# Kernel tuning notes

Hardware: AMD Instinct MI355X
Metric: run time of the kernel (lower is better)

The kernel has to match this reference:

```python
import jax, jax.numpy as jnp
import numpy as np

NUM_CLUSTER = 64
NUM_HEAD = 8
EMBED = 512
B, L = 32, 256
H = EMBED // NUM_HEAD  # 64


def setup_inputs() -> dict:
    key = jax.random.key(0)
    ks = jax.random.split(key, 8)
    inputs = jax.random.normal(ks[0], (B, L, EMBED), dtype=jnp.float32)
    emissions = jax.random.normal(ks[1], (B, L, NUM_CLUSTER), dtype=jnp.float32)
    targets = jax.random.randint(ks[2], (B, L), 0, NUM_CLUSTER)
    masks = jnp.ones((B, L), dtype=bool)
    scale = 1.0 / np.sqrt(H)
    W1 = jax.random.normal(ks[3], (NUM_CLUSTER, H), dtype=jnp.float32) * scale
    b1 = jax.random.normal(ks[4], (NUM_CLUSTER,), dtype=jnp.float32) * 0.01
    W2 = jax.random.normal(ks[5], (NUM_CLUSTER, H), dtype=jnp.float32) * scale
    b2 = jax.random.normal(ks[6], (NUM_CLUSTER,), dtype=jnp.float32) * 0.01
    start_transitions = jax.random.uniform(ks[7], (NUM_CLUSTER,), minval=-0.1, maxval=0.1, dtype=jnp.float32)
    end_transitions = jax.random.uniform(jax.random.fold_in(key, 99), (NUM_CLUSTER,), minval=-0.1, maxval=0.1, dtype=jnp.float32)
    return {"inputs": inputs, "emissions": emissions, "targets": targets, "masks": masks,
            "W1": W1, "b1": b1, "W2": W2, "b2": b2,
            "start_transitions": start_transitions, "end_transitions": end_transitions}


def reference(inputs, emissions, targets, masks, W1, b1, W2, b2, start_transitions, end_transitions):
    # batch_first -> time-major (L, B, ...)
    x = jnp.transpose(inputs, (1, 0, 2))          # [L,B,D]
    em = jnp.transpose(emissions, (1, 0, 2))      # [L,B,K]
    tg = targets.T                                # [L,B]
    mk = masks.T                                  # [L,B] bool
    Ls, Bs, D = x.shape
    K = start_transitions.shape[0]

    # biaffine per-step transitions: [L,B,K,K]
    flat = x.reshape(Ls, Bs, NUM_HEAD, D // NUM_HEAD)        # [L,B,C,H]
    e1 = jnp.einsum('lbch,kh->lbck', flat, W1) + b1          # [L,B,C,K]
    e2 = jnp.einsum('lbch,kh->lbck', flat, W2) + b2
    T = jnp.einsum('lbck,lbcj->lbkj', e1, e2)                # sum over channels

    mf = mk.astype(em.dtype)
    barange = jnp.arange(Bs)

    # ---- numerator (gold path score) ----
    score = start_transitions[tg[0]] + em[0, barange, tg[0]]
    steps = jnp.arange(1, Ls)[:, None]                       # [L-1,1]
    trans_sel = T[steps, barange[None, :], tg[:-1], tg[1:]]  # [L-1,B]
    em_sel = em[steps, barange[None, :], tg[1:]]             # [L-1,B]
    score = score + jnp.sum((trans_sel + em_sel) * mf[1:], axis=0)
    seq_ends = mk.astype(jnp.int32).sum(axis=0) - 1
    last_tags = tg[seq_ends, barange]
    numerator = score + end_transitions[last_tags]

    # ---- denominator (log partition) via scan ----
    def step(s, inp):
        Ti, emi, mki = inp                                   # [B,K,K],[B,K],[B]
        nxt = jax.nn.logsumexp(s[:, :, None] + Ti + emi[:, None, :], axis=1)
        s = jnp.where(mki[:, None], nxt, s)
        return s, None

    s0 = start_transitions + em[0]                           # [B,K]
    sF, _ = jax.lax.scan(step, s0, (T[1:], em[1:], mk[1:]))
    denominator = jax.nn.logsumexp(sF + end_transitions, axis=1)

    return numerator - denominator
```

## Files before the change

### kernel.cpp

```cpp
#include <hip/hip_runtime.h>
#include <hip/hip_bf16.h>
#include <cstddef>
#include <cstdint>

constexpr int Bn = 32;
constexpr int Ln = 256;
constexpr int SCH = 16;
constexpr int NCH = 16;

using bf16 = __hip_bfloat16;
typedef __bf16 bfv8 __attribute__((ext_vector_type(8)));
typedef float f32x16 __attribute__((ext_vector_type(16)));

union FragU {
  bfv8 f;
  uint4 q;
  uint2 d[2];
  unsigned short u[8];
};

__device__ inline unsigned int packbf2(float a, float b) {
  unsigned short lo = __builtin_bit_cast(unsigned short, __float2bfloat16(a));
  unsigned short hi = __builtin_bit_cast(unsigned short, __float2bfloat16(b));
  return (unsigned int)lo | ((unsigned int)hi << 16);
}
__device__ inline float bfbits2f(unsigned short v) {
  return __builtin_bit_cast(float, ((unsigned int)v) << 16);
}

__global__ __launch_bounds__(256) void chunk_kernel(
    const float* __restrict__ x, const float* __restrict__ W1,
    const float* __restrict__ b1, const float* __restrict__ W2,
    const float* __restrict__ b2, const float* __restrict__ em,
    const int* __restrict__ tg, bf16* __restrict__ cM,
    float* __restrict__ cOff, float* __restrict__ pnum) {
  const int blk = blockIdx.x;
  const int b = blk & (Bn - 1);
  const int c = blk >> 5;
  const int tid = threadIdx.x;
  const int lane = tid & 63;
  const int wv = tid >> 6;
  const int l31 = lane & 31, h5 = lane >> 5;

  __shared__ __align__(16) unsigned short smem[34816];
  __shared__ __align__(16) float ems[SCH * 64];
  __shared__ float wvoff[4], w2off[2];

  unsigned short* e1s = smem;
  unsigned short* e2s = smem + 8192;

  const int t0g = c * SCH;

  {
    const float4* src = (const float4*)(em + ((size_t)b * Ln + t0g) * 64);
    ((float4*)ems)[tid] = src[tid];
  }

  FragU fxa[4];
  {
    const float* xbase = x + ((size_t)(b * Ln + t0g)) * 512;
    const int m = wv * 32 + l31;
    const float* xrow = xbase + (size_t)(m >> 3) * 512 + (m & 7) * 64;
#pragma unroll
    for (int kb = 0; kb < 4; ++kb) {
      const float4 x0 = *(const float4*)(xrow + kb * 16 + h5 * 8);
      const float4 x1 = *(const float4*)(xrow + kb * 16 + h5 * 8 + 4);
      fxa[kb].d[0] = make_uint2(packbf2(x0.x, x0.y), packbf2(x0.z, x0.w));
      fxa[kb].d[1] = make_uint2(packbf2(x1.x, x1.y), packbf2(x1.z, x1.w));
    }
  }
#pragma unroll
  for (int arr = 0; arr < 2; ++arr) {
    const float* W = arr ? W2 : W1;
    const float* bb = arr ? b2 : b1;
    unsigned short* es = arr ? e2s : e1s;
#pragma unroll
    for (int nt = 0; nt < 2; ++nt) {
      const int k = nt * 32 + l31;
      f32x16 acc;
#pragma unroll
      for (int r = 0; r < 16; ++r) acc[r] = 0.f;
#pragma unroll
      for (int kb = 0; kb < 4; ++kb) {
        FragU fb;
        const float* wp = W + (size_t)k * 64 + kb * 16 + h5 * 8;
        const float4 w0 = *(const float4*)wp;
        const float4 w1 = *(const float4*)(wp + 4);
        fb.d[0] = make_uint2(packbf2(w0.x, w0.y), packbf2(w0.z, w0.w));
        fb.d[1] = make_uint2(packbf2(w1.x, w1.y), packbf2(w1.z, w1.w));
        acc = __builtin_amdgcn_mfma_f32_32x32x16_bf16(fxa[kb].f, fb.f, acc, 0, 0, 0);
      }
      const float bias = bb[k];
#pragma unroll
      for (int g = 0; g < 4; ++g) {
        const int tt = wv * 4 + g;
        const unsigned int lo = packbf2(acc[4 * g + 0] + bias, acc[4 * g + 1] + bias);
        const unsigned int hi = packbf2(acc[4 * g + 2] + bias, acc[4 * g + 3] + bias);
        *(uint2*)&es[tt * 512 + k * 8 + 4 * h5] = make_uint2(lo, hi);
      }
    }
  }
  __syncthreads();

  FragU f1[4][2], f2[4][2];
#pragma unroll
  for (int g = 0; g < 4; ++g)
#pragma unroll
    for (int a = 0; a < 2; ++a) {
      f1[g][a].q = make_uint4(0, 0, 0, 0);
      f2[g][a].q = make_uint4(0, 0, 0, 0);
      if (h5 == 0) {
        f1[g][a].q = *(const uint4*)&e1s[(4 * wv + g) * 512 + (a * 32 + l31) * 8];
        f2[g][a].q = *(const uint4*)&e2s[(4 * wv + g) * 512 + (a * 32 + l31) * 8];
      }
    }

  if (tid < 16) {
    const int tglob = t0g + tid;
    float part = 0.f;
    if (tglob >= 1) {
      const int kp = tg[b * Ln + tglob - 1];
      const int jc = tg[b * Ln + tglob];
      const unsigned short* p1 = &e1s[tid * 512 + kp * 8];
      const unsigned short* p2 = &e2s[tid * 512 + jc * 8];
      float tr = 0.f;
#pragma unroll
      for (int cc = 0; cc < 8; ++cc) tr += bfbits2f(p1[cc]) * bfbits2f(p2[cc]);
      part = tr + ems[tid * 64 + jc];
    }
#pragma unroll
    for (int o = 1; o < 16; o <<= 1) part += __shfl_xor(part, o);
    if (tid == 0) pnum[c * Bn + b] = part;
  }

  __syncthreads();

  unsigned short* A = smem + wv * 8704;
  unsigned short* Bs = A + 4352;

  auto wmax4 = [&](const f32x16& v0, const f32x16& v1, const f32x16& v2,
                   const f32x16& v3) -> float {
    float mx = v0[0];
#pragma unroll
    for (int r = 0; r < 16; ++r) {
      mx = fmaxf(mx, v0[r]); mx = fmaxf(mx, v1[r]);
      mx = fmaxf(mx, v2[r]); mx = fmaxf(mx, v3[r]);
    }
#pragma unroll
    for (int o = 1; o < 64; o <<= 1) mx = fmaxf(mx, __shfl_xor(mx, o));
    return mx;
  };

  auto stExp = [&](unsigned short* dst, const f32x16& v, int a2, int b2,
                   float sh) {
    unsigned short* d = &dst[(b2 * 32 + l31) * 68 + a2 * 32 + 4 * h5];
#pragma unroll
    for (int g = 0; g < 4; ++g) {
      const unsigned int lo =
          packbf2(__expf(v[4 * g + 0] - sh), __expf(v[4 * g + 1] - sh));
      const unsigned int hi =
          packbf2(__expf(v[4 * g + 2] - sh), __expf(v[4 * g + 3] - sh));
      *(uint2*)(d + 8 * g) = make_uint2(lo, hi);
    }
  };
  auto stScl = [&](unsigned short* dst, const f32x16& v, int a2, int b2,
                   float inv) {
    unsigned short* d = &dst[(b2 * 32 + l31) * 68 + a2 * 32 + 4 * h5];
#pragma unroll
    for (int g = 0; g < 4; ++g) {
      const unsigned int lo = packbf2(v[4 * g + 0] * inv, v[4 * g + 1] * inv);
      const unsigned int hi = packbf2(v[4 * g + 2] * inv, v[4 * g + 3] * inv);
      *(uint2*)(d + 8 * g) = make_uint2(lo, hi);
    }
  };

  auto computeP_R = [&](const FragU (&fe1)[2], const FragU (&fe2)[2], int tt,
                        unsigned short* dst) -> float {
    f32x16 c00, c01, c10, c11;
#pragma unroll
    for (int r = 0; r < 16; ++r) {
      const int rm = 4 * h5 + (r & 3) + 8 * (r >> 2);
      const float e0 = ems[tt * 64 + rm];
      const float e1v = ems[tt * 64 + 32 + rm];
      c00[r] = e0; c01[r] = e0; c10[r] = e1v; c11[r] = e1v;
    }
    c00 = __builtin_amdgcn_mfma_f32_32x32x16_bf16(fe2[0].f, fe1[0].f, c00, 0, 0, 0);
    c01 = __builtin_amdgcn_mfma_f32_32x32x16_bf16(fe2[0].f, fe1[1].f, c01, 0, 0, 0);
    c10 = __builtin_amdgcn_mfma_f32_32x32x16_bf16(fe2[1].f, fe1[0].f, c10, 0, 0, 0);
    c11 = __builtin_amdgcn_mfma_f32_32x32x16_bf16(fe2[1].f, fe1[1].f, c11, 0, 0, 0);
    const float mx = wmax4(c00, c01, c10, c11);
    stExp(dst, c00, 0, 0, mx);
    stExp(dst, c01, 0, 1, mx);
    stExp(dst, c10, 1, 0, mx);
    stExp(dst, c11, 1, 1, mx);
    return mx;
  };

  auto computeP_T = [&](const FragU (&fe1)[2], const FragU (&fe2)[2], int tt,
                        unsigned short* dst) -> float {
    const float emv0 = ems[tt * 64 + l31];
    const float emv1 = ems[tt * 64 + 32 + l31];
    f32x16 c00, c01, c10, c11;
#pragma unroll
    for (int r = 0; r < 16; ++r) {
      c00[r] = emv0; c01[r] = emv1; c10[r] = emv0; c11[r] = emv1;
    }
    c00 = __builtin_amdgcn_mfma_f32_32x32x16_bf16(fe1[0].f, fe2[0].f, c00, 0, 0, 0);
    c01 = __builtin_amdgcn_mfma_f32_32x32x16_bf16(fe1[0].f, fe2[1].f, c01, 0, 0, 0);
    c10 = __builtin_amdgcn_mfma_f32_32x32x16_bf16(fe1[1].f, fe2[0].f, c10, 0, 0, 0);
    c11 = __builtin_amdgcn_mfma_f32_32x32x16_bf16(fe1[1].f, fe2[1].f, c11, 0, 0, 0);
    const float mx = wmax4(c00, c01, c10, c11);
    stExp(dst, c00, 0, 0, mx);
    stExp(dst, c01, 0, 1, mx);
    stExp(dst, c10, 1, 0, mx);
    stExp(dst, c11, 1, 1, mx);
    return mx;
  };

  auto foldProd = [&](unsigned short* Adst, const unsigned short* Bsrc,
                      bool outT) -> float {
    const unsigned short* X = outT ? Adst : Bsrc;
    const unsigned short* Y = outT ? Bsrc : Adst;
    f32x16 a00, a01, a10, a11;
#pragma unroll
    for (int r = 0; r < 16; ++r) {
      a00[r] = 0.f; a01[r] = 0.f; a10[r] = 0.f; a11[r] = 0.f;
    }
#pragma unroll
    for (int kb = 0; kb < 4; ++kb) {
      const int koff = kb * 16 + h5 * 8;
      FragU x0, x1, y0, y1;
      const unsigned short* px0 = &X[l31 * 68 + koff];
      const unsigned short* px1 = &X[(32 + l31) * 68 + koff];
      const unsigned short* py0 = &Y[l31 * 68 + koff];
      const unsigned short* py1 = &Y[(32 + l31) * 68 + koff];
      x0.d[0] = *(const uint2*)px0;  x0.d[1] = *(const uint2*)(px0 + 4);
      x1.d[0] = *(const uint2*)px1;  x1.d[1] = *(const uint2*)(px1 + 4);
      y0.d[0] = *(const uint2*)py0;  y0.d[1] = *(const uint2*)(py0 + 4);
      y1.d[0] = *(const uint2*)py1;  y1.d[1] = *(const uint2*)(py1 + 4);
      a00 = __builtin_amdgcn_mfma_f32_32x32x16_bf16(x0.f, y0.f, a00, 0, 0, 0);
      a01 = __builtin_amdgcn_mfma_f32_32x32x16_bf16(x0.f, y1.f, a01, 0, 0, 0);
      a10 = __builtin_amdgcn_mfma_f32_32x32x16_bf16(x1.f, y0.f, a10, 0, 0, 0);
      a11 = __builtin_amdgcn_mfma_f32_32x32x16_bf16(x1.f, y1.f, a11, 0, 0, 0);
    }
    float mx = wmax4(a00, a01, a10, a11);
    mx = fmaxf(mx, 1e-30f);
    const float inv = 1.0f / mx;
    stScl(Adst, a00, 0, 0, inv);
    stScl(Adst, a01, 0, 1, inv);
    stScl(Adst, a10, 1, 0, inv);
    stScl(Adst, a11, 1, 1, inv);
    return __logf(mx);
  };

  float woff = 0.f;
  const int tstart = (c == 0 && wv == 0) ? 1 : 0;
  bool inited = false;
#pragma unroll
  for (int s = 0; s < 4; ++s) {
    if (s < tstart) continue;
    const int tt = 4 * wv + s;
    if (!inited) {
      woff += computeP_R(f1[s], f2[s], tt, A);
      inited = true;
    } else {
      woff += computeP_T(f1[s], f2[s], tt, Bs);
      woff += foldProd(A, Bs, (s == 3) && ((wv & 1) != 0));
    }
  }
  if (lane == 0) wvoff[wv] = woff;
  __syncthreads();

  if (wv == 0) {
    const float lm = foldProd(smem, smem + 8704, false);
    if (lane == 0) w2off[0] = wvoff[0] + wvoff[1] + lm;
  } else if (wv == 1) {
    const float lm = foldProd(smem + 2 * 8704, smem + 3 * 8704, true);
    if (lane == 0) w2off[1] = wvoff[2] + wvoff[3] + lm;
  }
  __syncthreads();

  if (wv == 0) {
    const float lm = foldProd(smem, smem + 2 * 8704, (c & 1) != 0);
    if (lane == 0) cOff[c * Bn + b] = w2off[0] + w2off[1] + lm;
  }
  __syncthreads();

  bf16* om = cM + ((size_t)(c * Bn + b)) * 4096;
#pragma unroll
  for (int pass = 0; pass < 4; ++pass) {
    const int e = pass * 1024 + tid * 4;
    const int i = e >> 6, j = e & 63;
    *(uint2*)((unsigned short*)om + e) = *(const uint2*)&smem[i * 68 + j];
  }
}

__global__ __launch_bounds__(256) void combine_kernel(
    const float* __restrict__ em, const int* __restrict__ tg,
    const float* __restrict__ st, const float* __restrict__ en,
    const bf16* __restrict__ cM, const float* __restrict__ cOff,
    const float* __restrict__ pnum, float* __restrict__ out) {
  const int b = blockIdx.x, tid = threadIdx.x;
  const int lane = tid & 63, wv = tid >> 6;
  const int l31 = lane & 31, h5 = lane >> 5;

  __shared__ __align__(16) unsigned short slots[8 * 4352];
  __shared__ float sexs[64];
  __shared__ float toff[8], toff2[4];
  __shared__ float num_s, den_s;

  float s0e = 0.f, env = 0.f, coffv = 0.f, pnv = 0.f;
  int tg0 = 0, tgl = 0;
  if (wv == 0) {
    s0e = __expf(st[lane] + em[(size_t)b * Ln * 64 + lane]);
    env = __expf(en[lane]);
    if (lane < 16) coffv = cOff[lane * Bn + b];
  } else if (wv == 1) {
    if (lane < 16) pnv = pnum[lane * Bn + b];
    if (lane == 0) {
      tg0 = tg[b * Ln];
      tgl = tg[b * Ln + Ln - 1];
    }
  }

  auto wmax4 = [&](const f32x16& v0, const f32x16& v1, const f32x16& v2,
                   const f32x16& v3) -> float {
    float mx = v0[0];
#pragma unroll
    for (int r = 0; r < 16; ++r) {
      mx = fmaxf(mx, v0[r]); mx = fmaxf(mx, v1[r]);
      mx = fmaxf(mx, v2[r]); mx = fmaxf(mx, v3[r]);
    }
#pragma unroll
    for (int o = 1; o < 64; o <<= 1) mx = fmaxf(mx, __shfl_xor(mx, o));
    return mx;
  };

  auto stTile = [&](unsigned short* dst, const f32x16& v, int i2, int j2,
                    float inv) {
    unsigned short* d = &dst[(j2 * 32 + l31) * 68 + i2 * 32 + 4 * h5];
#pragma unroll
    for (int g = 0; g < 4; ++g) {
      const unsigned int lo = packbf2(v[4 * g + 0] * inv, v[4 * g + 1] * inv);
      const unsigned int hi = packbf2(v[4 * g + 2] * inv, v[4 * g + 3] * inv);
      *(uint2*)(d + 8 * g) = make_uint2(lo, hi);
    }
  };

  auto prodL1 = [&](int pr) -> float {
    const unsigned short* Ag =
        (const unsigned short*)(cM + ((size_t)((2 * pr) * Bn + b)) * 4096);
    const unsigned short* Bg =
        (const unsigned short*)(cM + ((size_t)((2 * pr + 1) * Bn + b)) * 4096);
    const bool outT = (pr & 1) != 0;
    const unsigned short* X = outT ? Ag : Bg;
    const unsigned short* Y = outT ? Bg : Ag;
    f32x16 a00, a01, a10, a11;
#pragma unroll
    for (int r = 0; r < 16; ++r) {
      a00[r] = 0.f; a01[r] = 0.f; a10[r] = 0.f; a11[r] = 0.f;
    }
#pragma unroll
    for (int kb = 0; kb < 4; ++kb) {
      const int koff = kb * 16 + h5 * 8;
      FragU x0, x1, y0, y1;
      x0.q = *(const uint4*)&X[l31 * 64 + koff];
      x1.q = *(const uint4*)&X[(32 + l31) * 64 + koff];
      y0.q = *(const uint4*)&Y[l31 * 64 + koff];
      y1.q = *(const uint4*)&Y[(32 + l31) * 64 + koff];
      a00 = __builtin_amdgcn_mfma_f32_32x32x16_bf16(x0.f, y0.f, a00, 0, 0, 0);
      a01 = __builtin_amdgcn_mfma_f32_32x32x16_bf16(x0.f, y1.f, a01, 0, 0, 0);
      a10 = __builtin_amdgcn_mfma_f32_32x32x16_bf16(x1.f, y0.f, a10, 0, 0, 0);
      a11 = __builtin_amdgcn_mfma_f32_32x32x16_bf16(x1.f, y1.f, a11, 0, 0, 0);
    }
    float mx = wmax4(a00, a01, a10, a11);
    mx = fmaxf(mx, 1e-30f);
    const float inv = 1.0f / mx;
    unsigned short* dst = slots + pr * 4352;
    stTile(dst, a00, 0, 0, inv);
    stTile(dst, a01, 0, 1, inv);
    stTile(dst, a10, 1, 0, inv);
    stTile(dst, a11, 1, 1, inv);
    return __logf(mx);
  };

  auto prodL2 = [&](int q) -> float {
    const unsigned short* Xs = slots + (2 * q + 1) * 4352;
    const unsigned short* Ys = slots + (2 * q) * 4352;
    f32x16 a00, a01, a10, a11;
#pragma unroll
    for (int r = 0; r < 16; ++r) {
      a00[r] = 0.f; a01[r] = 0.f; a10[r] = 0.f; a11[r] = 0.f;
    }
#pragma unroll
    for (int kb = 0; kb < 4; ++kb) {
      const int koff = kb * 16 + h5 * 8;
      FragU x0, x1, y0, y1;
      const unsigned short* px0 = &Xs[l31 * 68 + koff];
      const unsigned short* px1 = &Xs[(32 + l31) * 68 + koff];
      const unsigned short* py0 = &Ys[l31 * 68 + koff];
      const unsigned short* py1 = &Ys[(32 + l31) * 68 + koff];
      x0.d[0] = *(const uint2*)px0;  x0.d[1] = *(const uint2*)(px0 + 4);
      x1.d[0] = *(const uint2*)px1;  x1.d[1] = *(const uint2*)(px1 + 4);
      y0.d[0] = *(const uint2*)py0;  y0.d[1] = *(const uint2*)(py0 + 4);
      y1.d[0] = *(const uint2*)py1;  y1.d[1] = *(const uint2*)(py1 + 4);
      a00 = __builtin_amdgcn_mfma_f32_32x32x16_bf16(x0.f, y0.f, a00, 0, 0, 0);
      a01 = __builtin_amdgcn_mfma_f32_32x32x16_bf16(x0.f, y1.f, a01, 0, 0, 0);
      a10 = __builtin_amdgcn_mfma_f32_32x32x16_bf16(x1.f, y0.f, a10, 0, 0, 0);
      a11 = __builtin_amdgcn_mfma_f32_32x32x16_bf16(x1.f, y1.f, a11, 0, 0, 0);
    }
    float mx = wmax4(a00, a01, a10, a11);
    mx = fmaxf(mx, 1e-30f);
    const float inv = 1.0f / mx;
    unsigned short* dst = slots + (2 * q) * 4352;
    stTile(dst, a00, 0, 0, inv);
    stTile(dst, a01, 0, 1, inv);
    stTile(dst, a10, 1, 0, inv);
    stTile(dst, a11, 1, 1, inv);
    return __logf(mx);
  };

#pragma unroll
  for (int pp = 0; pp < 2; ++pp) {
    const int pr = wv + pp * 4;
    const float lm = prodL1(pr);
    if (lane == 0) toff[pr] = lm;
  }
  __syncthreads();

  {
    const float child = toff[2 * wv] + toff[2 * wv + 1];
    const float lm2 = prodL2(wv);
    if (lane == 0) toff2[wv] = child + lm2;
  }
  __syncthreads();

  if (wv == 0) {
    float u = s0e;
#pragma unroll
    for (int f = 0; f < 4; ++f) {
      sexs[lane] = u;
      float acc2 = 0.f;
      const unsigned short* Mp = slots + (2 * f) * 4352;
#pragma unroll 8
      for (int k = 0; k < 64; ++k)
        acc2 += sexs[k] * bfbits2f(Mp[k * 68 + lane]);
      u = acc2;
    }
    const float w = u * env;
    float sg = w;
#pragma unroll
    for (int o = 1; o < 64; o <<= 1) sg += __shfl_xor(sg, o);
#pragma unroll
    for (int o = 1; o < 16; o <<= 1) coffv += __shfl_xor(coffv, o);
    if (lane == 0) {
      const float toffsum = toff2[0] + toff2[1] + toff2[2] + toff2[3];
      den_s = coffv + toffsum + __logf(sg);
    }
  } else if (wv == 1) {
    float nsum = pnv;
#pragma unroll
    for (int o = 1; o < 16; o <<= 1) nsum += __shfl_xor(nsum, o);
    if (lane == 0)
      num_s = nsum + st[tg0] + em[(size_t)b * Ln * 64 + tg0] + en[tgl];
  }
  __syncthreads();
  if (tid == 0) out[b] = num_s - den_s;
}

extern "C" void kernel_launch(void* const* d_in, const int* in_sizes, int n_in,
                              void* d_out, int out_size, void* d_ws, size_t ws_size,
                              hipStream_t stream) {
  const float* inputs    = (const float*)d_in[0];
  const float* emissions = (const float*)d_in[1];
  const int*   targets   = (const int*)d_in[2];
  const float* W1 = (const float*)d_in[4];
  const float* b1 = (const float*)d_in[5];
  const float* W2 = (const float*)d_in[6];
  const float* b2 = (const float*)d_in[7];
  const float* st = (const float*)d_in[8];
  const float* en = (const float*)d_in[9];
  float* outp = (float*)d_out;

  bf16* cM = (bf16*)d_ws;
  float* cOff = (float*)(cM + (size_t)NCH * Bn * 4096);
  float* pnum = cOff + NCH * Bn;

  chunk_kernel<<<dim3(NCH * Bn), dim3(256), 0, stream>>>(
      inputs, W1, b1, W2, b2, emissions, targets, cM, cOff, pnum);
  combine_kernel<<<dim3(Bn), dim3(256), 0, stream>>>(
      emissions, targets, st, en, cM, cOff, pnum, outp);
}
```

Baseline: 116.3 us.

## Reduce chunk matrices with a full MFMA product tree instead of serial matvecs

The combine kernel used to fold the four level-2 matrices into the state with four dependent 64-wide matrix-vector passes on a single wave. It now extends the matrix product tree by two more levels using MFMA (two waves, then one), with a transpose flag that keeps operand layouts consistent, and finishes with one matvec. It also sets a minimum of two blocks per CU on chunk_kernel through launch bounds. The cost is extra sync barriers and serial MFMA levels on fewer waves, plus possible register pressure in chunk_kernel.

New measurement: 114.8 us (median of 2 runs). About the same (-1.3%).

```diff
diff --git a/kernel.cpp b/kernel.cpp
--- a/kernel.cpp
+++ b/kernel.cpp
@@ -28,7 +28,7 @@
   return __builtin_bit_cast(float, ((unsigned int)v) << 16);
 }
 
-__global__ __launch_bounds__(256) void chunk_kernel(
+__global__ __launch_bounds__(256, 2) void chunk_kernel(
     const float* __restrict__ x, const float* __restrict__ W1,
     const float* __restrict__ b1, const float* __restrict__ W2,
     const float* __restrict__ b2, const float* __restrict__ em,
@@ -306,14 +306,15 @@
 
   __shared__ __align__(16) unsigned short slots[8 * 4352];
   __shared__ float sexs[64];
-  __shared__ float toff[8], toff2[4];
+  __shared__ float t1s[8], t2s[4], t3s[2];
   __shared__ float num_s, den_s;
 
-  float s0e = 0.f, env = 0.f, coffv = 0.f, pnv = 0.f;
+  float env = 0.f, coffv = 0.f, pnv = 0.f;
   int tg0 = 0, tgl = 0;
   if (wv == 0) {
-    s0e = __expf(st[lane] + em[(size_t)b * Ln * 64 + lane]);
+    const float s0e = __expf(st[lane] + em[(size_t)b * Ln * 64 + lane]);
     env = __expf(en[lane]);
+    sexs[lane] = s0e;
     if (lane < 16) coffv = cOff[lane * Bn + b];
   } else if (wv == 1) {
     if (lane < 16) pnv = pnum[lane * Bn + b];
@@ -384,9 +385,11 @@
     return __logf(mx);
   };
 
-  auto prodL2 = [&](int q) -> float {
-    const unsigned short* Xs = slots + (2 * q + 1) * 4352;
-    const unsigned short* Ys = slots + (2 * q) * 4352;
+  auto prodLDS = [&](int aSlot, int bSlot, bool outT) -> float {
+    const unsigned short* As = slots + aSlot * 4352;
+    const unsigned short* Bsr = slots + bSlot * 4352;
+    const unsigned short* X = outT ? As : Bsr;
+    const unsigned short* Y = outT ? Bsr : As;
     f32x16 a00, a01, a10, a11;
 #pragma unroll
     for (int r = 0; r < 16; ++r) {
@@ -396,10 +399,10 @@
     for (int kb = 0; kb < 4; ++kb) {
       const int koff = kb * 16 + h5 * 8;
       FragU x0, x1, y0, y1;
-      const unsigned short* px0 = &Xs[l31 * 68 + koff];
-      const unsigned short* px1 = &Xs[(32 + l31) * 68 + koff];
-      const unsigned short* py0 = &Ys[l31 * 68 + koff];
-      const unsigned short* py1 = &Ys[(32 + l31) * 68 + koff];
+      const unsigned short* px0 = &X[l31 * 68 + koff];
+      const unsigned short* px1 = &X[(32 + l31) * 68 + koff];
+      const unsigned short* py0 = &Y[l31 * 68 + koff];
+      const unsigned short* py1 = &Y[(32 + l31) * 68 + koff];
       x0.d[0] = *(const uint2*)px0;  x0.d[1] = *(const uint2*)(px0 + 4);
       x1.d[0] = *(const uint2*)px1;  x1.d[1] = *(const uint2*)(px1 + 4);
       y0.d[0] = *(const uint2*)py0;  y0.d[1] = *(const uint2*)(py0 + 4);
@@ -412,7 +415,7 @@
     float mx = wmax4(a00, a01, a10, a11);
     mx = fmaxf(mx, 1e-30f);
     const float inv = 1.0f / mx;
-    unsigned short* dst = slots + (2 * q) * 4352;
+    unsigned short* dst = slots + aSlot * 4352;
     stTile(dst, a00, 0, 0, inv);
     stTile(dst, a01, 0, 1, inv);
     stTile(dst, a10, 1, 0, inv);
@@ -424,39 +427,35 @@
   for (int pp = 0; pp < 2; ++pp) {
     const int pr = wv + pp * 4;
     const float lm = prodL1(pr);
-    if (lane == 0) toff[pr] = lm;
+    if (lane == 0) t1s[pr] = lm;
   }
   __syncthreads();
 
   {
-    const float child = toff[2 * wv] + toff[2 * wv + 1];
-    const float lm2 = prodL2(wv);
-    if (lane == 0) toff2[wv] = child + lm2;
+    const float lm = prodLDS(2 * wv, 2 * wv + 1, (wv & 1) != 0);
+    if (lane == 0) t2s[wv] = t1s[2 * wv] + t1s[2 * wv + 1] + lm;
+  }
+  __syncthreads();
+
+  if (wv < 2) {
+    const float lm = prodLDS(4 * wv, 4 * wv + 2, (wv & 1) != 0);
+    if (lane == 0) t3s[wv] = t2s[2 * wv] + t2s[2 * wv + 1] + lm;
   }
   __syncthreads();
 
   if (wv == 0) {
-    float u = s0e;
-#pragma unroll
-    for (int f = 0; f < 4; ++f) {
-      sexs[lane] = u;
-      float acc2 = 0.f;
-      const unsigned short* Mp = slots + (2 * f) * 4352;
+    const float lm4 = prodLDS(0, 4, false);
+    float acc2 = 0.f;
 #pragma unroll 8
-      for (int k = 0; k < 64; ++k)
-        acc2 += sexs[k] * bfbits2f(Mp[k * 68 + lane]);
-      u = acc2;
-    }
-    const float w = u * env;
+    for (int k = 0; k < 64; ++k)
+      acc2 += sexs[k] * bfbits2f(slots[k * 68 + lane]);
+    const float w = acc2 * env;
     float sg = w;
 #pragma unroll
     for (int o = 1; o < 64; o <<= 1) sg += __shfl_xor(sg, o);
 #pragma unroll
     for (int o = 1; o < 16; o <<= 1) coffv += __shfl_xor(coffv, o);
-    if (lane == 0) {
-      const float toffsum = toff2[0] + toff2[1] + toff2[2] + toff2[3];
-      den_s = coffv + toffsum + __logf(sg);
-    }
+    if (lane == 0) den_s = coffv + t3s[0] + t3s[1] + lm4 + __logf(sg);
   } else if (wv == 1) {
     float nsum = pnv;
 #pragma unroll
```
